# Performance work log

Measured on AMD Instinct MI355X. Metric: run time of the kernel, lower is better.

## Reference

```python
import jax, jax.numpy as jnp
import numpy as np

B, T, D, H, L = 2048, 512, 8, 20, 10  # batch, seq, input_dim, hidden_dim, num_layers


def setup_inputs() -> dict:
    key = jax.random.key(0)
    ks = jax.random.split(key, 10)
    s = 1.0 / np.sqrt(H)  # PyTorch nn.RNN / nn.Linear init bound
    u = lambda k, shape: jax.random.uniform(k, shape, jnp.float32, -s, s)
    return {
        "x": jax.random.normal(ks[0], (B, T, D), jnp.float32),
        "w_ih0": u(ks[1], (H, D)),        # layer-0 input weights
        "w_ih": u(ks[2], (L - 1, H, H)),  # layers 1..9 input weights
        "w_hh": u(ks[3], (L, H, H)),
        "b_ih": u(ks[4], (L, H)),
        "b_hh": u(ks[5], (L, H)),
        "fc_w": u(ks[6], (H, H)),
        "fc_b": u(ks[7], (H,)),
        "l2_w": u(ks[8], (1, H)),
        "l2_b": u(ks[9], (1,)),
    }


def reference(x, w_ih0, w_ih, w_hh, b_ih, b_hh, fc_w, fc_b, l2_w, l2_b):
    # 10-layer Elman RNN (tanh), batch_first, h0 = 0, eval mode (no dropout).
    Bn = x.shape[0]
    h0 = jnp.zeros((L, Bn, H), x.dtype)

    def step(h, x_t):  # h: [L, B, H], x_t: [B, D]
        hs = []
        inp = x_t
        for l in range(L):  # fixed small layer count -> unrolled
            Wi = w_ih0 if l == 0 else w_ih[l - 1]
            hl = jnp.tanh(inp @ Wi.T + b_ih[l] + h[l] @ w_hh[l].T + b_hh[l])
            hs.append(hl)
            inp = hl
        return jnp.stack(hs), hl  # carry, top-layer output

    _, out = jax.lax.scan(step, h0, jnp.swapaxes(x, 0, 1))  # out: [T, B, H]
    out = jnp.swapaxes(out, 0, 1)  # [B, T, H]
    # Time-independent MLP head (original loops over t; batched here, same math)
    y = jax.nn.relu(out @ fc_w.T + fc_b) @ l2_w.T + l2_b  # [B, T, 1]
    return y
```

## Files before the change

### kernel.cpp

```cpp
#include <hip/hip_runtime.h>

#if __has_builtin(__builtin_amdgcn_exp2f)
#define EXP2F(x) __builtin_amdgcn_exp2f(x)
#else
#define EXP2F(x) exp2f(x)
#endif
#if __has_builtin(__builtin_amdgcn_rcpf)
#define RCPF(x) __builtin_amdgcn_rcpf(x)
#else
#define RCPF(x) (1.0f / (x))
#endif

namespace {

constexpr int B_ = 2048, T_ = 512, D_ = 8, H_ = 20, L_ = 10;
constexpr int NG    = 16;
constexpr int PADK  = 40;
constexpr int NW    = 11;
constexpr int NTHR  = NW * 64;
constexpr int DEPTH = 4;
constexpr int SLOT_STRIDE  = L_ * NG * PADK;
constexpr int LAYER_STRIDE = NG * PADK;

typedef float f32x4 __attribute__((ext_vector_type(4)));
typedef short s16x8 __attribute__((ext_vector_type(8)));

#define LD4(p) (*reinterpret_cast<const f32x4*>(p))

__device__ __forceinline__ unsigned short f2bf(float f) {
    unsigned u = __builtin_bit_cast(unsigned, f);
    return (unsigned short)((u + 0x7FFFu + ((u >> 16) & 1u)) >> 16);
}
__device__ __forceinline__ float bf2f(unsigned short b) {
    return __builtin_bit_cast(float, (unsigned)b << 16);
}
__device__ __forceinline__ unsigned cvt_pk_bf16(float s0, float s1) {
    unsigned r;
    asm("v_cvt_pk_bf16_f32 %0, %1, %2" : "=v"(r) : "v"(s0), "v"(s1));
    return r;
}

__device__ __forceinline__ f32x4 mfma_bf16(s16x8 a, s16x8 b, f32x4 c) {
    return __builtin_amdgcn_mfma_f32_16x16x32_bf16(a, b, c, 0, 0, 0);
}

__device__ __forceinline__ float tanh_fast(float x) {
    float e = EXP2F(x * 2.8853900817779268f);
    return fmaf(-2.0f, RCPF(1.0f + e), 1.0f);
}

__device__ __forceinline__ void wait_ge(int* p, int v) {
    while (__hip_atomic_load(p, __ATOMIC_ACQUIRE,
                             __HIP_MEMORY_SCOPE_WORKGROUP) < v) {}
    __builtin_amdgcn_sched_barrier(0);
}

__device__ __forceinline__ void publish(int* p, int v) {
    asm volatile("s_waitcnt lgkmcnt(0)" ::: "memory");
    __hip_atomic_store(p, v, __ATOMIC_RELAXED, __HIP_MEMORY_SCOPE_WORKGROUP);
}

__global__ __launch_bounds__(NTHR) void rnn_async(
    const float* __restrict__ x,
    const float* __restrict__ w_ih0,
    const float* __restrict__ w_ih,
    const float* __restrict__ w_hh,
    const float* __restrict__ b_ih,
    const float* __restrict__ b_hh,
    const float* __restrict__ fc_w,
    const float* __restrict__ fc_b,
    const float* __restrict__ l2_w,
    const float* __restrict__ l2_b,
    float* __restrict__ out)
{
    __shared__ __align__(16) unsigned short h_lds[DEPTH][L_][NG][PADK];
    __shared__ int prog[16];

    const int tid = threadIdx.x;
    const int w   = tid >> 6;
    const int l   = tid & 63;
    const int col = l & 15;
    const int g   = l >> 4;
    const int bg  = blockIdx.x * NG;

    {
        uint4* p4 = reinterpret_cast<uint4*>(&h_lds[0][0][0][0]);
        const int n4 = DEPTH * L_ * NG * PADK / 8;
        for (int i = tid; i < n4; i += NTHR) p4[i] = make_uint4(0, 0, 0, 0);
        if (tid < 16) prog[tid] = 0;
    }

    s16x8 a0_hi = {0,0,0,0,0,0,0,0}, a0_lo = a0_hi, a1_hi = a0_hi, a1_lo = a0_hi;
    s16x8 h0_hi = a0_hi, h0_lo = a0_hi, h1_hi = a0_hi, h1_lo = a0_hi;
    f32x4 bias0 = {0.f, 0.f, 0.f, 0.f}, bias1 = bias0;
    f32x4 l2v0 = bias0, l2v1 = bias0;
    float l2bv = 0.f;
    const bool mt1ok = col < (H_ - 16);

    if (w < L_) {
        const int layer = w;
        #pragma unroll
        for (int e = 0; e < 8; ++e) {
            const int k = g * 8 + e;
            float wv0 = 0.f, wv1 = 0.f;
            if (layer == 0) {
                if (k < 16) {
                    wv0 = w_ih0[col * D_ + (k & 7)];
                    if (mt1ok) wv1 = w_ih0[(16 + col) * D_ + (k & 7)];
                }
            } else if (k < H_) {
                wv0 = w_ih[((layer - 1) * H_ + col) * H_ + k];
                if (mt1ok) wv1 = w_ih[((layer - 1) * H_ + 16 + col) * H_ + k];
            }
            unsigned short b0 = f2bf(wv0), b1 = f2bf(wv1);
            a0_hi[e] = (short)b0; a0_lo[e] = (short)f2bf(wv0 - bf2f(b0));
            a1_hi[e] = (short)b1; a1_lo[e] = (short)f2bf(wv1 - bf2f(b1));
            float uv0 = 0.f, uv1 = 0.f;
            if (k < H_) {
                uv0 = w_hh[(layer * H_ + col) * H_ + k];
                if (mt1ok) uv1 = w_hh[(layer * H_ + 16 + col) * H_ + k];
            }
            unsigned short c0 = f2bf(uv0), c1 = f2bf(uv1);
            h0_hi[e] = (short)c0; h0_lo[e] = (short)f2bf(uv0 - bf2f(c0));
            h1_hi[e] = (short)c1; h1_lo[e] = (short)f2bf(uv1 - bf2f(c1));
        }
        #pragma unroll
        for (int r = 0; r < 4; ++r) {
            const int row = g * 4 + r;
            bias0[r] = b_ih[layer * H_ + row] + b_hh[layer * H_ + row];
            bias1[r] = (g == 0) ? (b_ih[layer * H_ + 16 + r] +
                                   b_hh[layer * H_ + 16 + r]) : 0.f;
        }
    } else {
        #pragma unroll
        for (int e = 0; e < 8; ++e) {
            const int k = g * 8 + e;
            float f0 = 0.f, f1 = 0.f;
            if (k < H_) {
                f0 = fc_w[col * H_ + k];
                if (mt1ok) f1 = fc_w[(16 + col) * H_ + k];
            }
            unsigned short b0 = f2bf(f0), b1 = f2bf(f1);
            a0_hi[e] = (short)b0; a0_lo[e] = (short)f2bf(f0 - bf2f(b0));
            a1_hi[e] = (short)b1; a1_lo[e] = (short)f2bf(f1 - bf2f(b1));
        }
        #pragma unroll
        for (int r = 0; r < 4; ++r) {
            bias0[r] = fc_b[g * 4 + r];
            bias1[r] = (g == 0) ? fc_b[16 + r] : 0.f;
            l2v0[r]  = l2_w[g * 4 + r];
            l2v1[r]  = (g == 0) ? l2_w[16 + r] : 0.f;
        }
        l2bv = l2_b[0];
    }

    f32x4 xq0a = {0.f,0.f,0.f,0.f}, xq0b = xq0a;
    f32x4 xq1a = xq0a, xq1b = xq0a, xq2a = xq0a, xq2b = xq0a;
    if (w == 0 && g < 2) {
        const float* xp = x + (size_t)(bg + col) * T_ * D_;
        xq0a = LD4(xp);          xq0b = LD4(xp + 4);
        xq1a = LD4(xp + D_);     xq1b = LD4(xp + D_ + 4);
        xq2a = LD4(xp + 2 * D_); xq2b = LD4(xp + 2 * D_ + 4);
    }

    __syncthreads();

    unsigned short* const hb = &h_lds[0][0][0][0];
    const f32x4 z4 = {0.f, 0.f, 0.f, 0.f};

    if (w < L_) {
        const int rdB1 = w * LAYER_STRIDE + col * PADK + g * 8;
        const int rdB0 = (w ? (w - 1) * LAYER_STRIDE : 0) + col * PADK + g * 8;
        const int wr0  = w * LAYER_STRIDE + col * PADK + g * 4;
        const int wr1  = w * LAYER_STRIDE + col * PADK + 16;
        for (int t = 0; t < T_; ++t) {
            const int s_cur = (t & 3) * SLOT_STRIDE;
            const int s_prv = ((t + 3) & 3) * SLOT_STRIDE;
            s16x8 B1 = *reinterpret_cast<const s16x8*>(hb + s_prv + rdB1);
            s16x8 B0;
            if (w == 0) {
                s16x8 xf = {0,0,0,0,0,0,0,0};
                if (g < 2) {
                    #pragma unroll
                    for (int e = 0; e < 8; ++e) {
                        float f = (e < 4) ? xq0a[e] : xq0b[e - 4];
                        unsigned short hbit = f2bf(f);
                        xf[e] = (short)((g == 0) ? hbit : f2bf(f - bf2f(hbit)));
                    }
                    xq0a = xq1a; xq0b = xq1b;
                    xq1a = xq2a; xq1b = xq2b;
                    if (t + 3 < T_) {
                        const float* xp = x + ((size_t)(bg + col) * T_ + t + 3) * D_;
                        xq2a = LD4(xp); xq2b = LD4(xp + 4);
                    }
                }
                B0 = xf;
            } else {
                wait_ge(&prog[w - 1], t + 1);
                B0 = *reinterpret_cast<const s16x8*>(hb + s_cur + rdB0);
            }
            f32x4 A  = mfma_bf16(h0_hi, B1, bias0);
            f32x4 Ab = mfma_bf16(h0_lo, B1, z4);
            f32x4 C  = mfma_bf16(h1_hi, B1, bias1);
            f32x4 Cb = mfma_bf16(h1_lo, B1, z4);
            A  = mfma_bf16(a0_hi, B0, A);
            Ab = mfma_bf16(a0_lo, B0, Ab);
            C  = mfma_bf16(a1_hi, B0, C);
            Cb = mfma_bf16(a1_lo, B0, Cb);
            f32x4 acc0 = A + Ab, acc1 = C + Cb;
            uint2 pw;
            pw.x = cvt_pk_bf16(tanh_fast(acc0[0]), tanh_fast(acc0[1]));
            pw.y = cvt_pk_bf16(tanh_fast(acc0[2]), tanh_fast(acc0[3]));
            uint2 qw = make_uint2(0u, 0u);
            if (g == 0) {
                qw.x = cvt_pk_bf16(tanh_fast(acc1[0]), tanh_fast(acc1[1]));
                qw.y = cvt_pk_bf16(tanh_fast(acc1[2]), tanh_fast(acc1[3]));
            }
            if (t >= DEPTH) wait_ge(&prog[w + 1], t - (DEPTH - 1));
            *reinterpret_cast<uint2*>(hb + s_cur + wr0) = pw;
            if (g == 0)
                *reinterpret_cast<uint2*>(hb + s_cur + wr1) = qw;
            if (l == 0) publish(&prog[w], t + 1);
        }
    } else {
        const int rdH = (L_ - 1) * LAYER_STRIDE + col * PADK + g * 8;
        for (int t = 0; t < T_; ++t) {
            wait_ge(&prog[L_ - 1], t + 1);
            s16x8 Bh = *reinterpret_cast<const s16x8*>(
                hb + (t & 3) * SLOT_STRIDE + rdH);
            f32x4 z0  = mfma_bf16(a0_hi, Bh, bias0);
            f32x4 z0b = mfma_bf16(a0_lo, Bh, z4);
            f32x4 z1  = mfma_bf16(a1_hi, Bh, bias1);
            f32x4 z1b = mfma_bf16(a1_lo, Bh, z4);
            z0 += z0b; z1 += z1b;
            float part = 0.f;
            #pragma unroll
            for (int r = 0; r < 4; ++r) {
                part = fmaf(l2v0[r], fmaxf(z0[r], 0.f), part);
                part = fmaf(l2v1[r], fmaxf(z1[r], 0.f), part);
            }
            part += __shfl_xor(part, 16);
            part += __shfl_xor(part, 32);
            if (l < NG) out[(size_t)(bg + l) * T_ + t] = part + l2bv;
            if (l == 0) publish(&prog[L_], t + 1);
        }
    }
}

}

extern "C" void kernel_launch(void* const* d_in, const int* in_sizes, int n_in,
                              void* d_out, int out_size, void* d_ws, size_t ws_size,
                              hipStream_t stream) {
    const float* x     = (const float*)d_in[0];
    const float* w_ih0 = (const float*)d_in[1];
    const float* w_ih  = (const float*)d_in[2];
    const float* w_hh  = (const float*)d_in[3];
    const float* b_ih  = (const float*)d_in[4];
    const float* b_hh  = (const float*)d_in[5];
    const float* fc_w  = (const float*)d_in[6];
    const float* fc_b  = (const float*)d_in[7];
    const float* l2_w  = (const float*)d_in[8];
    const float* l2_b  = (const float*)d_in[9];
    float* out = (float*)d_out;

    const int grid = B_ / NG;
    hipLaunchKernelGGL(rnn_async, dim3(grid), dim3(NTHR), 0, stream,
                       x, w_ih0, w_ih, w_hh, b_ih, b_hh, fc_w, fc_b,
                       l2_w, l2_b, out);
}
```

Baseline: 361.1 us.

## Feed recurrent state via wave shuffles, defer LDS publish, deepen ring buffer

Each layer wave now rebuilds its own recurrent MFMA operand from the previous step's packed outputs using cross-lane shuffles, so the recurrent read no longer goes through LDS. The LDS write and progress publish for step t-1 are moved to the start of step t, and the ring depth goes from 4 to 8 slots. Progress counters are cached so spin loads are skipped when a neighbour is already far enough ahead. The x input is converted to bf16 hi/lo one step ahead. Together these aim to shorten the per-step critical path and reduce stalls between pipelined layer waves, at the cost of more LDS, extra shuffles, and a later publish that downstream layers must wait for.

```diff
diff --git a/kernel.cpp b/kernel.cpp
--- a/kernel.cpp
+++ b/kernel.cpp
@@ -18,12 +18,13 @@
 constexpr int PADK  = 40;
 constexpr int NW    = 11;
 constexpr int NTHR  = NW * 64;
-constexpr int DEPTH = 4;
+constexpr int DEPTH = 8;
 constexpr int SLOT_STRIDE  = L_ * NG * PADK;
 constexpr int LAYER_STRIDE = NG * PADK;
 
 typedef float f32x4 __attribute__((ext_vector_type(4)));
 typedef short s16x8 __attribute__((ext_vector_type(8)));
+typedef unsigned u32x4 __attribute__((ext_vector_type(4)));
 
 #define LD4(p) (*reinterpret_cast<const f32x4*>(p))
 
@@ -39,25 +40,35 @@
     asm("v_cvt_pk_bf16_f32 %0, %1, %2" : "=v"(r) : "v"(s0), "v"(s1));
     return r;
 }
-
 __device__ __forceinline__ f32x4 mfma_bf16(s16x8 a, s16x8 b, f32x4 c) {
     return __builtin_amdgcn_mfma_f32_16x16x32_bf16(a, b, c, 0, 0, 0);
 }
-
 __device__ __forceinline__ float tanh_fast(float x) {
     float e = EXP2F(x * 2.8853900817779268f);
     return fmaf(-2.0f, RCPF(1.0f + e), 1.0f);
 }
 
-__device__ __forceinline__ void wait_ge(int* p, int v) {
-    while (__hip_atomic_load(p, __ATOMIC_ACQUIRE,
-                             __HIP_MEMORY_SCOPE_WORKGROUP) < v) {}
+__device__ __forceinline__ int wait_ge_ret(int* p, int v) {
+    int cur = __hip_atomic_load(p, __ATOMIC_ACQUIRE, __HIP_MEMORY_SCOPE_WORKGROUP);
+    while (cur < v)
+        cur = __hip_atomic_load(p, __ATOMIC_ACQUIRE, __HIP_MEMORY_SCOPE_WORKGROUP);
     __builtin_amdgcn_sched_barrier(0);
-}
-
+    return cur;
+}
 __device__ __forceinline__ void publish(int* p, int v) {
     asm volatile("s_waitcnt lgkmcnt(0)" ::: "memory");
     __hip_atomic_store(p, v, __ATOMIC_RELAXED, __HIP_MEMORY_SCOPE_WORKGROUP);
+}
+
+__device__ __forceinline__ s16x8 pack_x(f32x4 a, f32x4 b, bool lo) {
+    s16x8 r;
+    #pragma unroll
+    for (int e = 0; e < 8; ++e) {
+        float f = (e < 4) ? a[e] : b[e - 4];
+        unsigned short hb = f2bf(f);
+        r[e] = (short)(lo ? f2bf(f - bf2f(hb)) : hb);
+    }
+    return r;
 }
 
 __global__ __launch_bounds__(NTHR) void rnn_async(
@@ -154,13 +165,14 @@
         l2bv = l2_b[0];
     }
 
-    f32x4 xq0a = {0.f,0.f,0.f,0.f}, xq0b = xq0a;
-    f32x4 xq1a = xq0a, xq1b = xq0a, xq2a = xq0a, xq2b = xq0a;
+    const int i0 = (g == 1) ? col + 32 : col;
+    const int i1 = (g == 0) ? col + 16 : ((g == 1) ? col + 48 : col);
+
+    s16x8 xf_cur = {0,0,0,0,0,0,0,0}, xf_nxt = xf_cur;
     if (w == 0 && g < 2) {
         const float* xp = x + (size_t)(bg + col) * T_ * D_;
-        xq0a = LD4(xp);          xq0b = LD4(xp + 4);
-        xq1a = LD4(xp + D_);     xq1b = LD4(xp + D_ + 4);
-        xq2a = LD4(xp + 2 * D_); xq2b = LD4(xp + 2 * D_ + 4);
+        xf_cur = pack_x(LD4(xp), LD4(xp + 4), g == 1);
+        xf_nxt = pack_x(LD4(xp + D_), LD4(xp + D_ + 4), g == 1);
     }
 
     __syncthreads();
@@ -169,35 +181,41 @@
     const f32x4 z4 = {0.f, 0.f, 0.f, 0.f};
 
     if (w < L_) {
-        const int rdB1 = w * LAYER_STRIDE + col * PADK + g * 8;
         const int rdB0 = (w ? (w - 1) * LAYER_STRIDE : 0) + col * PADK + g * 8;
         const int wr0  = w * LAYER_STRIDE + col * PADK + g * 4;
         const int wr1  = w * LAYER_STRIDE + col * PADK + 16;
+        uint2 pw = make_uint2(0u, 0u), qw = pw;
+        int p_up = 0, p_dn = 0;
         for (int t = 0; t < T_; ++t) {
-            const int s_cur = (t & 3) * SLOT_STRIDE;
-            const int s_prv = ((t + 3) & 3) * SLOT_STRIDE;
-            s16x8 B1 = *reinterpret_cast<const s16x8*>(hb + s_prv + rdB1);
+            unsigned s0 = __shfl(pw.x, i0), s1 = __shfl(pw.y, i0);
+            unsigned s2 = __shfl(pw.x, i1), s3 = __shfl(pw.y, i1);
+            unsigned u0 = __shfl(qw.x, col), u1 = __shfl(qw.y, col);
+            u32x4 bw;
+            bw[0] = (g < 2) ? s0 : ((g == 2) ? u0 : 0u);
+            bw[1] = (g < 2) ? s1 : ((g == 2) ? u1 : 0u);
+            bw[2] = (g < 2) ? s2 : 0u;
+            bw[3] = (g < 2) ? s3 : 0u;
+            s16x8 B1 = __builtin_bit_cast(s16x8, bw);
+            if (t > 0) {
+                const int sp = ((t - 1) & (DEPTH - 1)) * SLOT_STRIDE;
+                if (t - 1 >= DEPTH && p_dn < t - DEPTH)
+                    p_dn = wait_ge_ret(&prog[w + 1], t - DEPTH);
+                *reinterpret_cast<uint2*>(hb + sp + wr0) = pw;
+                if (g == 0) *reinterpret_cast<uint2*>(hb + sp + wr1) = qw;
+                if (l == 0) publish(&prog[w], t);
+            }
             s16x8 B0;
             if (w == 0) {
-                s16x8 xf = {0,0,0,0,0,0,0,0};
-                if (g < 2) {
-                    #pragma unroll
-                    for (int e = 0; e < 8; ++e) {
-                        float f = (e < 4) ? xq0a[e] : xq0b[e - 4];
-                        unsigned short hbit = f2bf(f);
-                        xf[e] = (short)((g == 0) ? hbit : f2bf(f - bf2f(hbit)));
-                    }
-                    xq0a = xq1a; xq0b = xq1b;
-                    xq1a = xq2a; xq1b = xq2b;
-                    if (t + 3 < T_) {
-                        const float* xp = x + ((size_t)(bg + col) * T_ + t + 3) * D_;
-                        xq2a = LD4(xp); xq2b = LD4(xp + 4);
-                    }
+                B0 = xf_cur;
+                xf_cur = xf_nxt;
+                if (g < 2 && t + 2 < T_) {
+                    const float* xp = x + ((size_t)(bg + col) * T_ + t + 2) * D_;
+                    xf_nxt = pack_x(LD4(xp), LD4(xp + 4), g == 1);
                 }
-                B0 = xf;
             } else {
-                wait_ge(&prog[w - 1], t + 1);
-                B0 = *reinterpret_cast<const s16x8*>(hb + s_cur + rdB0);
+                if (p_up < t + 1) p_up = wait_ge_ret(&prog[w - 1], t + 1);
+                B0 = *reinterpret_cast<const s16x8*>(
+                    hb + (t & (DEPTH - 1)) * SLOT_STRIDE + rdB0);
             }
             f32x4 A  = mfma_bf16(h0_hi, B1, bias0);
             f32x4 Ab = mfma_bf16(h0_lo, B1, z4);
@@ -208,26 +226,25 @@
             C  = mfma_bf16(a1_hi, B0, C);
             Cb = mfma_bf16(a1_lo, B0, Cb);
             f32x4 acc0 = A + Ab, acc1 = C + Cb;
-            uint2 pw;
             pw.x = cvt_pk_bf16(tanh_fast(acc0[0]), tanh_fast(acc0[1]));
             pw.y = cvt_pk_bf16(tanh_fast(acc0[2]), tanh_fast(acc0[3]));
-            uint2 qw = make_uint2(0u, 0u);
-            if (g == 0) {
-                qw.x = cvt_pk_bf16(tanh_fast(acc1[0]), tanh_fast(acc1[1]));
-                qw.y = cvt_pk_bf16(tanh_fast(acc1[2]), tanh_fast(acc1[3]));
-            }
-            if (t >= DEPTH) wait_ge(&prog[w + 1], t - (DEPTH - 1));
-            *reinterpret_cast<uint2*>(hb + s_cur + wr0) = pw;
-            if (g == 0)
-                *reinterpret_cast<uint2*>(hb + s_cur + wr1) = qw;
-            if (l == 0) publish(&prog[w], t + 1);
+            qw.x = cvt_pk_bf16(tanh_fast(acc1[0]), tanh_fast(acc1[1]));
+            qw.y = cvt_pk_bf16(tanh_fast(acc1[2]), tanh_fast(acc1[3]));
+        }
+        {
+            const int sp = ((T_ - 1) & (DEPTH - 1)) * SLOT_STRIDE;
+            if (p_dn < T_ - DEPTH) wait_ge_ret(&prog[w + 1], T_ - DEPTH);
+            *reinterpret_cast<uint2*>(hb + sp + wr0) = pw;
+            if (g == 0) *reinterpret_cast<uint2*>(hb + sp + wr1) = qw;
+            if (l == 0) publish(&prog[w], T_);
         }
     } else {
         const int rdH = (L_ - 1) * LAYER_STRIDE + col * PADK + g * 8;
+        int p_up = 0;
         for (int t = 0; t < T_; ++t) {
-            wait_ge(&prog[L_ - 1], t + 1);
+            if (p_up < t + 1) p_up = wait_ge_ret(&prog[L_ - 1], t + 1);
             s16x8 Bh = *reinterpret_cast<const s16x8*>(
-                hb + (t & 3) * SLOT_STRIDE + rdH);
+                hb + (t & (DEPTH - 1)) * SLOT_STRIDE + rdH);
             f32x4 z0  = mfma_bf16(a0_hi, Bh, bias0);
             f32x4 z0b = mfma_bf16(a0_lo, Bh, z4);
             f32x4 z1  = mfma_bf16(a1_hi, Bh, bias1);
```

Result: slower. 368.7 us (+2.1%).
